# Optimization experiments

Hardware: AMD Instinct MI355X
Metric: run time of the kernel (lower is better)

## Reference

```python
import jax, jax.numpy as jnp
import numpy as np

N, E, T, H, O, L = 8192, 262144, 256, 2048, 1024, 128


def setup_inputs() -> dict:
    key = jax.random.key(0)
    ks = jax.random.split(key, 24)
    inp = {}
    inp["eeg_nodes"] = jax.random.normal(ks[0], (N, T), dtype=jnp.float32)
    inp["eeg_idx"] = jax.random.randint(ks[1], (2, E), 0, N, dtype=jnp.int32)
    # PyG models.GIN layer widths: [T->2048], [2048->2048], [2048->2048], [2048->1024]
    dims = [(T, H), (H, H), (H, H), (H, O)]
    k = 2
    for l, (din, dh) in enumerate(dims):
        inp[f"w1_{l}"] = jax.random.normal(ks[k], (din, dh), jnp.float32) / np.float32(np.sqrt(din)); k += 1
        inp[f"b1_{l}"] = jnp.zeros((dh,), jnp.float32)
        inp[f"w2_{l}"] = jax.random.normal(ks[k], (dh, dh), jnp.float32) / np.float32(np.sqrt(dh)); k += 1
        inp[f"b2_{l}"] = jnp.zeros((dh,), jnp.float32)
    inp["wm"] = jax.random.normal(ks[k], (O, L), jnp.float32) / np.float32(np.sqrt(O)); k += 1
    inp["bm"] = jnp.zeros((L,), jnp.float32)
    inp["wv"] = jax.random.normal(ks[k], (O, L), jnp.float32) / np.float32(np.sqrt(O)); k += 1
    inp["bv"] = jnp.zeros((L,), jnp.float32)
    # reparameterize noise (torch.randn_like) made explicit for determinism
    inp["eps"] = jax.random.normal(ks[k + 1], (N, L), jnp.float32)
    return inp


def _gin_conv(x, src, dst, w1, b1, w2, b2):
    # GINConv, eps=0: mlp((1+0)*x + sum_{j->i} x_j); MLP = Linear-ReLU-Linear (no norm)
    agg = jax.ops.segment_sum(x[src], dst, num_segments=x.shape[0])  # [N, d]
    h = jax.nn.relu((x + agg) @ w1 + b1)
    return h @ w2 + b2


def reference(eeg_nodes, eeg_idx, w1_0, b1_0, w2_0, b2_0, w1_1, b1_1, w2_1, b2_1,
              w1_2, b1_2, w2_2, b2_2, w1_3, b1_3, w2_3, b2_3, wm, bm, wv, bv, eps):
    src, dst = eeg_idx[0], eeg_idx[1]
    layers = [(w1_0, b1_0, w2_0, b2_0), (w1_1, b1_1, w2_1, b2_1),
              (w1_2, b1_2, w2_2, b2_2), (w1_3, b1_3, w2_3, b2_3)]
    x = eeg_nodes
    for i, (w1, b1, w2, b2) in enumerate(layers):
        x = _gin_conv(x, src, dst, w1, b1, w2, b2)
        if i < len(layers) - 1:  # BasicGNN: ReLU between convs, not after last
            x = jax.nn.relu(x)
    mean = x @ wm + bm
    var = x @ wv + bv
    z = mean + var * eps  # reparameterize
    return (z, mean, var)
```

## Files before the change

### kernel.cpp

```cpp
#include <hip/hip_runtime.h>

#define NN 8192
#define EE 262144
#define TT 256
#define HH 2048
#define OO 1024
#define LL 128
#define NW 10

typedef __bf16 bf16_t;
typedef __bf16 bf16x8_t __attribute__((ext_vector_type(8)));
typedef float f32x4_t __attribute__((ext_vector_type(4)));

__device__ __forceinline__ void async16(void* lds, const void* g) {
  __builtin_amdgcn_global_load_lds(
      (const __attribute__((address_space(1))) void*)g,
      (__attribute__((address_space(3))) void*)lds, 16, 0, 0);
}


__global__ __launch_bounds__(256) void count_deg_kernel(const int* __restrict__ dst,
                                                        int* __restrict__ deg) {
  int e = blockIdx.x * 256 + threadIdx.x;
  if (e < EE) atomicAdd(&deg[dst[e]], 1);
}

__global__ __launch_bounds__(1024) void scan_kernel(const int* __restrict__ deg,
                                                    int* __restrict__ rs) {
  __shared__ int s[1024];
  int t = threadIdx.x;
  int pre[8];
  int sum = 0;
#pragma unroll
  for (int j = 0; j < 8; ++j) { pre[j] = sum; sum += deg[t * 8 + j]; }
  s[t] = sum;
  __syncthreads();
  for (int off = 1; off < 1024; off <<= 1) {
    int add = (t >= off) ? s[t - off] : 0;
    __syncthreads();
    s[t] += add;
    __syncthreads();
  }
  int base = (t == 0) ? 0 : s[t - 1];
#pragma unroll
  for (int j = 0; j < 8; ++j) rs[t * 8 + j] = base + pre[j];
  if (t == 1023) rs[8192] = s[1023];
}

__global__ __launch_bounds__(256) void fill_csr_kernel(const int* __restrict__ src,
                                                       const int* __restrict__ dst,
                                                       const int* __restrict__ rs,
                                                       int* __restrict__ cur,
                                                       int* __restrict__ csr) {
  int e = blockIdx.x * 256 + threadIdx.x;
  if (e >= EE) return;
  int d = dst[e];
  int p = atomicAdd(&cur[d], 1);
  csr[rs[d] + p] = src[e];
}

struct WTab {
  const float* src[NW];
  int K[NW];
  int N[NW];
  long long dstOff[NW];
  int tileStart[NW + 1];
  const float* x0;
  bf16_t* castDst;
  int castStart;
};

__global__ __launch_bounds__(256) void prep_all_kernel(WTab tab, bf16_t* __restrict__ WT) {
  int b = blockIdx.x;
  int t = threadIdx.x;
  if (b >= tab.castStart) {
    int i = (b - tab.castStart) * 256 + t;
    f32x4_t a = ((const f32x4_t*)tab.x0)[i * 2];
    f32x4_t bb = ((const f32x4_t*)tab.x0)[i * 2 + 1];
    bf16x8_t o;
#pragma unroll
    for (int j = 0; j < 4; ++j) { o[j] = (bf16_t)a[j]; o[4 + j] = (bf16_t)bb[j]; }
    ((bf16x8_t*)tab.castDst)[i] = o;
    return;
  }
  int wi = 0;
#pragma unroll
  for (int k = 1; k < NW; ++k)
    if (b >= tab.tileStart[k]) wi = k;
  int tt = b - tab.tileStart[wi];
  int K = tab.K[wi], N = tab.N[wi];
  int ntn = N >> 6;
  int n0 = (tt % ntn) * 64, k0 = (tt / ntn) * 64;
  const float* in = tab.src[wi];
  bf16_t* out = WT + tab.dstOff[wi];

  __shared__ float tile[64][65];
  for (int c = t; c < 1024; c += 256) {
    int r = c >> 4, col = (c & 15) * 4;
    f32x4_t v = *(const f32x4_t*)&in[(size_t)(k0 + r) * N + n0 + col];
#pragma unroll
    for (int j = 0; j < 4; ++j) tile[r][col + j] = v[j];
  }
  __syncthreads();
  for (int c = t; c < 512; c += 256) {
    int r = c >> 3, col = (c & 7) * 8;
    bf16x8_t v;
#pragma unroll
    for (int j = 0; j < 8; ++j) v[j] = (bf16_t)tile[col + j][r];
    *(bf16x8_t*)&out[(size_t)(n0 + r) * K + k0 + col] = v;
  }
}

__global__ __launch_bounds__(256) void transpose_cast_kernel(const float* __restrict__ in,
                                                             bf16_t* __restrict__ out,
                                                             int K, int N) {
  __shared__ float tile[64][65];
  int n0 = blockIdx.x * 64, k0 = blockIdx.y * 64;
  int t = threadIdx.x;
  for (int c = t; c < 1024; c += 256) {
    int r = c >> 4, col = (c & 15) * 4;
    f32x4_t v = *(const f32x4_t*)&in[(size_t)(k0 + r) * N + n0 + col];
#pragma unroll
    for (int j = 0; j < 4; ++j) tile[r][col + j] = v[j];
  }
  __syncthreads();
  for (int c = t; c < 512; c += 256) {
    int r = c >> 3, col = (c & 7) * 8;
    bf16x8_t v;
#pragma unroll
    for (int j = 0; j < 8; ++j) v[j] = (bf16_t)tile[col + j][r];
    *(bf16x8_t*)&out[(size_t)(n0 + r) * K + k0 + col] = v;
  }
}

__global__ __launch_bounds__(256) void cast_kernel(const float* __restrict__ in,
                                                   bf16_t* __restrict__ out) {
  int i = blockIdx.x * 256 + threadIdx.x;
  f32x4_t a = ((const f32x4_t*)in)[i * 2];
  f32x4_t b = ((const f32x4_t*)in)[i * 2 + 1];
  bf16x8_t o;
#pragma unroll
  for (int j = 0; j < 4; ++j) { o[j] = (bf16_t)a[j]; o[4 + j] = (bf16_t)b[j]; }
  ((bf16x8_t*)out)[i] = o;
}

__global__ __launch_bounds__(64) void agg0_kernel(const bf16_t* __restrict__ x,
                                                  bf16_t* __restrict__ out,
                                                  const int* __restrict__ rs,
                                                  const int* __restrict__ csr) {
  int t = threadIdx.x;
  int node = blockIdx.x * 2 + (t >> 5);
  int c = t & 31;
  const bf16x8_t* xv = (const bf16x8_t*)x;
  bf16x8_t self = xv[(size_t)node * 32 + c];
  float acc[8];
#pragma unroll
  for (int j = 0; j < 8; ++j) acc[j] = (float)self[j];
  int e0 = rs[node], e1 = rs[node + 1];
  int e = e0;
  for (; e + 4 <= e1; e += 4) {
    int s0 = csr[e], s1 = csr[e + 1], s2 = csr[e + 2], s3 = csr[e + 3];
    bf16x8_t v0 = xv[(size_t)s0 * 32 + c];
    bf16x8_t v1 = xv[(size_t)s1 * 32 + c];
    bf16x8_t v2 = xv[(size_t)s2 * 32 + c];
    bf16x8_t v3 = xv[(size_t)s3 * 32 + c];
#pragma unroll
    for (int j = 0; j < 8; ++j)
      acc[j] += (float)v0[j] + (float)v1[j] + (float)v2[j] + (float)v3[j];
  }
  for (; e < e1; ++e) {
    bf16x8_t v = xv[(size_t)csr[e] * 32 + c];
#pragma unroll
    for (int j = 0; j < 8; ++j) acc[j] += (float)v[j];
  }
  bf16x8_t o;
#pragma unroll
  for (int j = 0; j < 8; ++j) o[j] = (bf16_t)acc[j];
  ((bf16x8_t*)out)[(size_t)node * 32 + c] = o;
}

__global__ __launch_bounds__(256) void agg_tiled_kernel(const bf16_t* __restrict__ x,
                                                        bf16_t* __restrict__ out,
                                                        const int* __restrict__ rs,
                                                        const int* __restrict__ csr,
                                                        const float* __restrict__ bias,
                                                        int relu, int tmask, int tshift) {
  int t = threadIdx.x;
  int tile = blockIdx.x & tmask;
  int ng = blockIdx.x >> tshift;
  int node = ng * 8 + (t >> 5);
  int c = t & 31;
  size_t tb = (size_t)tile * (NN * 32);
  const bf16x8_t* xv = (const bf16x8_t*)x + tb;
  bf16x8_t self = xv[node * 32 + c];
  float acc[8];
#pragma unroll
  for (int j = 0; j < 8; ++j) acc[j] = (float)self[j];
  int e0 = rs[node], e1 = rs[node + 1];
  int e = e0;
  for (; e + 4 <= e1; e += 4) {
    int s0 = csr[e], s1 = csr[e + 1], s2 = csr[e + 2], s3 = csr[e + 3];
    bf16x8_t v0 = xv[s0 * 32 + c];
    bf16x8_t v1 = xv[s1 * 32 + c];
    bf16x8_t v2 = xv[s2 * 32 + c];
    bf16x8_t v3 = xv[s3 * 32 + c];
#pragma unroll
    for (int j = 0; j < 8; ++j)
      acc[j] += (float)v0[j] + (float)v1[j] + (float)v2[j] + (float)v3[j];
  }
  for (; e < e1; ++e) {
    bf16x8_t v = xv[csr[e] * 32 + c];
#pragma unroll
    for (int j = 0; j < 8; ++j) acc[j] += (float)v[j];
  }
  if (bias) {
    const float* bp = bias + tile * 256 + c * 8;
    f32x4_t b0 = *(const f32x4_t*)bp;
    f32x4_t b1 = *(const f32x4_t*)(bp + 4);
#pragma unroll
    for (int j = 0; j < 4; ++j) { acc[j] += b0[j]; acc[4 + j] += b1[j]; }
  }
  if (relu) {
#pragma unroll
    for (int j = 0; j < 8; ++j) acc[j] = fmaxf(acc[j], 0.f);
  }
  bf16x8_t o;
#pragma unroll
  for (int j = 0; j < 8; ++j) o[j] = (bf16_t)acc[j];
  ((bf16x8_t*)out + tb)[node * 32 + c] = o;
}

template <int CMODE>
__global__ __launch_bounds__(256, 2) void gemm_bt_kernel(
    const bf16_t* __restrict__ A, const bf16_t* __restrict__ Bt,
    const float* __restrict__ bias, const float* __restrict__ biasB,
    void* __restrict__ Cv, int N, int K, int relu, int nbxShift) {
  __shared__ __align__(16) bf16_t lA[128 * 32];
  __shared__ __align__(16) bf16_t lB[128 * 32];
  const int tid = threadIdx.x;
  const int lane = tid & 63;
  const int wave = tid >> 6;
  const int wm64 = (wave & 1) * 64;
  const int wn64 = (wave >> 1) * 64;
  const int row16 = lane & 15;
  const int quad = lane >> 4;

  const int bid = blockIdx.x;
  const int xcd = bid & 7;
  const int rank = bid >> 3;
  const int bn = rank & ((1 << nbxShift) - 1);
  const int mPer = gridDim.x >> (3 + nbxShift);
  const int bm = xcd * mPer + (rank >> nbxShift);
  const size_t m0 = (size_t)bm * 128;
  const size_t n0 = (size_t)bn * 128;

  f32x4_t acc[4][4];
#pragma unroll
  for (int i = 0; i < 4; ++i)
#pragma unroll
    for (int j = 0; j < 4; ++j)
#pragma unroll
      for (int r = 0; r < 4; ++r) acc[i][j][r] = 0.f;

  const bf16_t* Bbase = Bt + n0 * K;
  const int r0 = tid >> 2;
  const int r1 = (tid + 256) >> 2;
  const int kc = (tid & 3) * 8;

  for (int kt = 0; kt < K; kt += 32) {
    const bf16_t* Ab = A + ((size_t)(kt >> 8)) * (NN * 256) + (kt & 255) + kc;
    async16(&lA[tid * 8], Ab + (m0 + r0) * 256);
    async16(&lA[(tid + 256) * 8], Ab + (m0 + r1) * 256);
    async16(&lB[tid * 8], Bbase + (size_t)r0 * K + kt + kc);
    async16(&lB[(tid + 256) * 8], Bbase + (size_t)r1 * K + kt + kc);
    __syncthreads();
    bf16x8_t af[4], bfr[4];
#pragma unroll
    for (int i = 0; i < 4; ++i)
      af[i] = *(const bf16x8_t*)&lA[(wm64 + i * 16 + row16) * 32 + quad * 8];
#pragma unroll
    for (int i = 0; i < 4; ++i)
      bfr[i] = *(const bf16x8_t*)&lB[(wn64 + i * 16 + row16) * 32 + quad * 8];
#pragma unroll
    for (int i = 0; i < 4; ++i)
#pragma unroll
      for (int j = 0; j < 4; ++j)
        acc[i][j] = __builtin_amdgcn_mfma_f32_16x16x32_bf16(af[i], bfr[j], acc[i][j], 0, 0, 0);
    __syncthreads();
  }

#pragma unroll
  for (int i = 0; i < 4; ++i) {
    size_t row = m0 + wm64 + i * 16 + quad * 4;
#pragma unroll
    for (int j = 0; j < 4; ++j) {
      int col = (int)n0 + wn64 + j * 16 + row16;
      if (CMODE == 0) {
        float b = bias ? bias[col] : 0.f;
        size_t cb = ((size_t)(col >> 8)) * (NN * 256) + (col & 255);
#pragma unroll
        for (int r = 0; r < 4; ++r) {
          float o = acc[i][j][r] + b;
          if (relu) o = fmaxf(o, 0.f);
          ((bf16_t*)Cv)[cb + (row + r) * 256] = (bf16_t)o;
        }
      } else {
        int sel = col >> 7;
        int c2 = col & 127;
        float b = sel ? biasB[c2] : bias[c2];
        float* dstp = (float*)Cv + (size_t)(1 + sel) * NN * LL + c2;
#pragma unroll
        for (int r = 0; r < 4; ++r) {
          dstp[(row + r) * LL] = acc[i][j][r] + b;
        }
      }
    }
  }
}

__global__ __launch_bounds__(256) void reparam_kernel(const float* __restrict__ mean,
                                                      const float* __restrict__ var,
                                                      const float* __restrict__ eps,
                                                      float* __restrict__ z) {
  int i = blockIdx.x * 256 + threadIdx.x;
  f32x4_t m = ((const f32x4_t*)mean)[i];
  f32x4_t v = ((const f32x4_t*)var)[i];
  f32x4_t e = ((const f32x4_t*)eps)[i];
  f32x4_t o;
#pragma unroll
  for (int j = 0; j < 4; ++j) o[j] = m[j] + v[j] * e[j];
  ((f32x4_t*)z)[i] = o;
}

extern "C" void kernel_launch(void* const* d_in, const int* in_sizes, int n_in,
                              void* d_out, int out_size, void* d_ws, size_t ws_size,
                              hipStream_t stream) {
  (void)in_sizes; (void)n_in; (void)out_size;
  const float* x0 = (const float*)d_in[0];
  const int* ei = (const int*)d_in[1];
  const int* src = ei;
  const int* dst = ei + EE;
  const float* w1[4] = {(const float*)d_in[2], (const float*)d_in[6],
                        (const float*)d_in[10], (const float*)d_in[14]};
  const float* b1[4] = {(const float*)d_in[3], (const float*)d_in[7],
                        (const float*)d_in[11], (const float*)d_in[15]};
  const float* w2[4] = {(const float*)d_in[4], (const float*)d_in[8],
                        (const float*)d_in[12], (const float*)d_in[16]};
  const float* b2[4] = {(const float*)d_in[5], (const float*)d_in[9],
                        (const float*)d_in[13], (const float*)d_in[17]};
  const float* wm = (const float*)d_in[18];
  const float* bm = (const float*)d_in[19];
  const float* wv = (const float*)d_in[20];
  const float* bv = (const float*)d_in[21];
  const float* eps = (const float*)d_in[22];
  float* out = (float*)d_out;

  char* ws = (char*)d_ws;
  bf16_t* B0 = (bf16_t*)(ws);
  bf16_t* B1 = (bf16_t*)(ws + 33554432);
  bf16_t* WT = (bf16_t*)(ws + 67108864);

  const long long soff[NW] = {0LL, 524288LL, 4718592LL, 8912896LL, 13107200LL,
                              17301504LL, 21495808LL, 23592960LL, 24641536LL, 24772608LL};
  const size_t wtBytesFull = 24903680ULL * 2ULL;
  const size_t needFull = 67108864ULL + wtBytesFull + 2097152ULL;
  bool full = ws_size >= needFull;

  size_t csrBase = full ? (67108864ULL + wtBytesFull) : 75497472ULL;
  int* deg = (int*)(ws + csrBase);
  int* cur = deg + 8192;
  int* rs = deg + 16384;
  int* csr = deg + 16384 + 8200;

  auto AGG = [&](const bf16_t* in, bf16_t* outp, int d, const float* bias, int relu) {
    int ntiles = d >> 8;
    int tshift = (ntiles == 8) ? 3 : 2;
    agg_tiled_kernel<<<(NN / 8) * ntiles, 256, 0, stream>>>(in, outp, rs, csr, bias, relu,
                                                            ntiles - 1, tshift);
  };

  if (full) {
    WTab tab;
    const float* srcs[NW] = {w1[0], w2[0], w1[1], w2[1], w1[2], w2[2], w1[3], w2[3], wm, wv};
    const int Ks[NW] = {TT, HH, HH, HH, HH, HH, HH, OO, OO, OO};
    const int Ns[NW] = {HH, HH, HH, HH, HH, HH, OO, OO, LL, LL};
    int cum = 0;
    for (int i = 0; i < NW; ++i) {
      tab.src[i] = srcs[i];
      tab.K[i] = Ks[i];
      tab.N[i] = Ns[i];
      tab.dstOff[i] = soff[i];
      tab.tileStart[i] = cum;
      cum += (Ns[i] >> 6) * (Ks[i] >> 6);
    }
    tab.tileStart[NW] = cum;
    tab.castStart = cum;
    tab.x0 = x0;
    tab.castDst = B0;
    int totalBlocks = cum + (NN * TT / 8) / 256;
    prep_all_kernel<<<totalBlocks, 256, 0, stream>>>(tab, WT);

    hipMemsetAsync(deg, 0, 2 * 8192 * sizeof(int), stream);
    count_deg_kernel<<<EE / 256, 256, 0, stream>>>(dst, deg);
    scan_kernel<<<1, 1024, 0, stream>>>(deg, rs);
    fill_csr_kernel<<<EE / 256, 256, 0, stream>>>(src, dst, rs, cur, csr);

    auto G = [&](const bf16_t* A, int wi, const float* bias, bf16_t* C, int Nn, int K, int relu) {
      int nbx = Nn / 128;
      int shift = __builtin_ctz(nbx);
      gemm_bt_kernel<0><<<nbx * (NN / 128), 256, 0, stream>>>(
          A, WT + soff[wi], bias, nullptr, (void*)C, Nn, K, relu, shift);
    };

    agg0_kernel<<<NN / 2, 64, 0, stream>>>(B0, B1, rs, csr);
    G(B1, 0, b1[0], B0, HH, TT, 1);
    G(B0, 1, b2[0], B1, HH, HH, 1);
    AGG(B1, B0, HH, nullptr, 0);
    G(B0, 2, b1[1], B1, HH, HH, 1);
    G(B1, 3, b2[1], B0, HH, HH, 1);
    AGG(B0, B1, HH, nullptr, 0);
    G(B1, 4, b1[2], B0, HH, HH, 1);
    G(B0, 5, b2[2], B1, HH, HH, 1);
    G(B1, 6, nullptr, B0, OO, HH, 0);
    AGG(B0, B1, OO, b1[3], 1);
    G(B1, 7, b2[3], B0, OO, OO, 0);
    gemm_bt_kernel<1><<<2 * (NN / 128), 256, 0, stream>>>(
        B0, WT + soff[8], bm, bv, (void*)out, 256, OO, 0, 1);
  } else {
    hipMemsetAsync(deg, 0, 2 * 8192 * sizeof(int), stream);
    count_deg_kernel<<<EE / 256, 256, 0, stream>>>(dst, deg);
    scan_kernel<<<1, 1024, 0, stream>>>(deg, rs);
    fill_csr_kernel<<<EE / 256, 256, 0, stream>>>(src, dst, rs, cur, csr);

    auto T = [&](const float* w, int K, int Nn, bf16_t* dstw) {
      transpose_cast_kernel<<<dim3(Nn / 64, K / 64), 256, 0, stream>>>(w, dstw, K, Nn);
    };
    auto G = [&](const bf16_t* A, const float* bias, bf16_t* C, int Nn, int K, int relu) {
      int nbx = Nn / 128;
      int shift = __builtin_ctz(nbx);
      gemm_bt_kernel<0><<<nbx * (NN / 128), 256, 0, stream>>>(
          A, WT, bias, nullptr, (void*)C, Nn, K, relu, shift);
    };

    cast_kernel<<<(NN * TT / 8) / 256, 256, 0, stream>>>(x0, B0);
    agg0_kernel<<<NN / 2, 64, 0, stream>>>(B0, B1, rs, csr);
    T(w1[0], TT, HH, WT); G(B1, b1[0], B0, HH, TT, 1);
    T(w2[0], HH, HH, WT); G(B0, b2[0], B1, HH, HH, 1);
    AGG(B1, B0, HH, nullptr, 0);
    T(w1[1], HH, HH, WT); G(B0, b1[1], B1, HH, HH, 1);
    T(w2[1], HH, HH, WT); G(B1, b2[1], B0, HH, HH, 1);
    AGG(B0, B1, HH, nullptr, 0);
    T(w1[2], HH, HH, WT); G(B1, b1[2], B0, HH, HH, 1);
    T(w2[2], HH, HH, WT); G(B0, b2[2], B1, HH, HH, 1);
    T(w1[3], HH, OO, WT); G(B1, nullptr, B0, OO, HH, 0);
    AGG(B0, B1, OO, b1[3], 1);
    T(w2[3], OO, OO, WT); G(B1, b2[3], B0, OO, OO, 0);
    T(wm, OO, LL, WT);
    T(wv, OO, LL, WT + (size_t)LL * OO);
    gemm_bt_kernel<1><<<2 * (NN / 128), 256, 0, stream>>>(
        B0, WT, bm, bv, (void*)out, 256, OO, 0, 1);
  }

  reparam_kernel<<<(NN * LL / 4) / 256, 256, 0, stream>>>(
      out + (size_t)NN * LL, out + (size_t)2 * NN * LL, eps, out);
}
```

Measured before the change: 874.2 us.

## Add 256x256-tile 8-wave GEMM with quadrant ping-pong for 2048-wide layers

Adds a new GEMM kernel that uses 256x256 output tiles with 512 threads, double-buffered LDS, and a four-quadrant schedule interleaving LDS fragment loads, async global-to-LDS staging and MFMA blocks with priority raising. It replaces the 128x128 GEMM for all six N=2048 layers. The aim is higher arithmetic intensity per loaded byte and better overlap of memory with matrix cores. In exchange it uses 128 KB of LDS per block, heavy register pressure, and a fine-grained barrier schedule whose correctness depends on precise vmcnt accounting.

```diff
diff --git a/kernel.cpp b/kernel.cpp
--- a/kernel.cpp
+++ b/kernel.cpp
@@ -316,6 +316,155 @@
       }
     }
   }
+}
+
+__global__ __launch_bounds__(512, 2) void gemm256_kernel(
+    const bf16_t* __restrict__ A, const bf16_t* __restrict__ Bt,
+    const float* __restrict__ bias, bf16_t* __restrict__ C,
+    int N, int K, int relu, int nbxShift) {
+  __shared__ __align__(16) bf16_t lA[2][256 * 64];
+  __shared__ __align__(16) bf16_t lB[2][256 * 64];
+
+  const int t = threadIdx.x;
+  const int lane = t & 63;
+  const int wave = t >> 6;
+  const int wm = wave >> 2;
+  const int wn = wave & 3;
+  const int row16 = lane & 15;
+  const int quad = lane >> 4;
+  const int sx = (row16 & 7) << 3;
+
+  const int r0 = t >> 3;
+  const int cs = ((t & 7) * 8) ^ ((r0 & 7) << 3);
+
+  const int bid = blockIdx.x;
+  const int xcd = bid & 7;
+  const int rank = bid >> 3;
+  const int bn = rank & ((1 << nbxShift) - 1);
+  const int mPer = gridDim.x >> (3 + nbxShift);
+  const int bm = xcd * mPer + (rank >> nbxShift);
+  const size_t m0 = (size_t)bm * 256;
+  const size_t n0 = (size_t)bn * 256;
+  const int NT = K >> 6;
+
+  f32x4_t acc[4][4][2];
+#pragma unroll
+  for (int Q = 0; Q < 4; ++Q)
+#pragma unroll
+    for (int i = 0; i < 4; ++i)
+#pragma unroll
+      for (int j = 0; j < 2; ++j)
+#pragma unroll
+        for (int r = 0; r < 4; ++r) acc[Q][i][j][r] = 0.f;
+
+  bf16x8_t af[4][2], bf[2][2];
+
+#define LOAD_A256(mh)                                                              \
+  _Pragma("unroll") for (int i = 0; i < 4; ++i)                                    \
+  _Pragma("unroll") for (int ks = 0; ks < 2; ++ks) {                               \
+    int row_ = (mh)*128 + wm * 64 + i * 16 + row16;                                \
+    af[i][ks] = *(const bf16x8_t*)&lA[c][row_ * 64 + ((ks * 32 + quad * 8) ^ sx)]; \
+  }
+
+#define LOAD_B256(nh)                                                              \
+  _Pragma("unroll") for (int j = 0; j < 2; ++j)                                    \
+  _Pragma("unroll") for (int ks = 0; ks < 2; ++ks) {                               \
+    int row_ = (nh)*128 + wn * 32 + j * 16 + row16;                                \
+    bf[j][ks] = *(const bf16x8_t*)&lB[c][row_ * 64 + ((ks * 32 + quad * 8) ^ sx)]; \
+  }
+
+#define STAGE_A256(U, mh)                                                            \
+  {                                                                                  \
+    int u_ = (U);                                                                    \
+    int us_ = u_ < NT ? u_ : NT - 1;                                                 \
+    int kt_ = us_ << 6;                                                              \
+    const bf16_t* g_ = A + (size_t)(kt_ >> 8) * (NN * 256) + (m0 + (mh)*128) * 256 + \
+                       (kt_ & 255) + cs;                                             \
+    bf16_t* l_ = &lA[u_ & 1][(mh)*8192];                                             \
+    async16(l_ + (size_t)t * 8, g_ + (size_t)r0 * 256);                              \
+    async16(l_ + (size_t)(t + 512) * 8, g_ + (size_t)(r0 + 64) * 256);               \
+  }
+
+#define STAGE_B256(U, nh)                                                  \
+  {                                                                        \
+    int u_ = (U);                                                          \
+    int us_ = u_ < NT ? u_ : NT - 1;                                       \
+    int kt_ = us_ << 6;                                                    \
+    const bf16_t* g_ = Bt + (n0 + (nh)*128) * (size_t)K + kt_ + cs;        \
+    bf16_t* l_ = &lB[u_ & 1][(nh)*8192];                                   \
+    async16(l_ + (size_t)t * 8, g_ + (size_t)r0 * K);                      \
+    async16(l_ + (size_t)(t + 512) * 8, g_ + (size_t)(r0 + 64) * K);       \
+  }
+
+#define MFMA_Q(Q)                                                                    \
+  __builtin_amdgcn_s_setprio(1);                                                     \
+  _Pragma("unroll") for (int i = 0; i < 4; ++i)                                      \
+  _Pragma("unroll") for (int j = 0; j < 2; ++j)                                      \
+  _Pragma("unroll") for (int ks = 0; ks < 2; ++ks)                                   \
+      acc[Q][i][j] =                                                                 \
+          __builtin_amdgcn_mfma_f32_16x16x32_bf16(af[i][ks], bf[j][ks], acc[Q][i][j],\
+                                                  0, 0, 0);                          \
+  __builtin_amdgcn_s_setprio(0);
+
+#define BAR asm volatile("s_barrier" ::: "memory")
+
+  STAGE_A256(0, 0); STAGE_B256(0, 0); STAGE_A256(0, 1); STAGE_B256(0, 1);
+  asm volatile("" ::: "memory");
+  STAGE_A256(1, 0); STAGE_B256(1, 0);
+  asm volatile("s_waitcnt vmcnt(4)" ::: "memory");
+  BAR;
+
+  for (int T = 0; T < NT; ++T) {
+    const int c = T & 1;
+    LOAD_A256(0); LOAD_B256(0);
+    STAGE_A256(T + 1, 1); STAGE_B256(T + 1, 1);
+    BAR;
+    MFMA_Q(0);
+    BAR;
+    LOAD_B256(1);
+    BAR;
+    MFMA_Q(1);
+    BAR;
+    LOAD_A256(1); LOAD_B256(0);
+    STAGE_A256(T + 2, 0);
+    BAR;
+    MFMA_Q(2);
+    BAR;
+    LOAD_B256(1);
+    STAGE_B256(T + 2, 0);
+    BAR;
+    MFMA_Q(3);
+    asm volatile("s_waitcnt vmcnt(4)" ::: "memory");
+    BAR;
+  }
+  asm volatile("s_waitcnt vmcnt(0)" ::: "memory");
+
+#pragma unroll
+  for (int Q = 0; Q < 4; ++Q) {
+    const int mh = Q >> 1, nh = Q & 1;
+#pragma unroll
+    for (int i = 0; i < 4; ++i) {
+      size_t row = m0 + mh * 128 + wm * 64 + i * 16 + quad * 4;
+#pragma unroll
+      for (int j = 0; j < 2; ++j) {
+        int col = (int)n0 + nh * 128 + wn * 32 + j * 16 + row16;
+        float b = bias ? bias[col] : 0.f;
+        size_t cb = ((size_t)(col >> 8)) * (NN * 256) + (col & 255);
+#pragma unroll
+        for (int r = 0; r < 4; ++r) {
+          float o = acc[Q][i][j][r] + b;
+          if (relu) o = fmaxf(o, 0.f);
+          C[cb + (row + r) * 256] = (bf16_t)o;
+        }
+      }
+    }
+  }
+#undef LOAD_A256
+#undef LOAD_B256
+#undef STAGE_A256
+#undef STAGE_B256
+#undef MFMA_Q
+#undef BAR
 }
 
 __global__ __launch_bounds__(256) void reparam_kernel(const float* __restrict__ mean,
@@ -405,22 +554,27 @@
     scan_kernel<<<1, 1024, 0, stream>>>(deg, rs);
     fill_csr_kernel<<<EE / 256, 256, 0, stream>>>(src, dst, rs, cur, csr);
 
-    auto G = [&](const bf16_t* A, int wi, const float* bias, bf16_t* C, int Nn, int K, int relu) {
+    auto G2 = [&](const bf16_t* Ain, int wi, const float* bias, bf16_t* Cout, int K, int relu) {
+      gemm256_kernel<<<8 * (NN / 256), 512, 0, stream>>>(Ain, WT + soff[wi], bias, Cout,
+                                                         HH, K, relu, 3);
+    };
+    auto G = [&](const bf16_t* Ain, int wi, const float* bias, bf16_t* Cout, int Nn, int K,
+                 int relu) {
       int nbx = Nn / 128;
       int shift = __builtin_ctz(nbx);
       gemm_bt_kernel<0><<<nbx * (NN / 128), 256, 0, stream>>>(
-          A, WT + soff[wi], bias, nullptr, (void*)C, Nn, K, relu, shift);
+          Ain, WT + soff[wi], bias, nullptr, (void*)Cout, Nn, K, relu, shift);
     };
 
     agg0_kernel<<<NN / 2, 64, 0, stream>>>(B0, B1, rs, csr);
-    G(B1, 0, b1[0], B0, HH, TT, 1);
-    G(B0, 1, b2[0], B1, HH, HH, 1);
+    G2(B1, 0, b1[0], B0, TT, 1);
+    G2(B0, 1, b2[0], B1, HH, 1);
     AGG(B1, B0, HH, nullptr, 0);
-    G(B0, 2, b1[1], B1, HH, HH, 1);
-    G(B1, 3, b2[1], B0, HH, HH, 1);
+    G2(B0, 2, b1[1], B1, HH, 1);
+    G2(B1, 3, b2[1], B0, HH, 1);
     AGG(B0, B1, HH, nullptr, 0);
-    G(B1, 4, b1[2], B0, HH, HH, 1);
-    G(B0, 5, b2[2], B1, HH, HH, 1);
+    G2(B1, 4, b1[2], B0, HH, 1);
+    G2(B0, 5, b2[2], B1, HH, 1);
     G(B1, 6, nullptr, B0, OO, HH, 0);
     AGG(B0, B1, OO, b1[3], 1);
     G(B1, 7, b2[3], B0, OO, OO, 0);
@@ -435,23 +589,26 @@
     auto T = [&](const float* w, int K, int Nn, bf16_t* dstw) {
       transpose_cast_kernel<<<dim3(Nn / 64, K / 64), 256, 0, stream>>>(w, dstw, K, Nn);
     };
-    auto G = [&](const bf16_t* A, const float* bias, bf16_t* C, int Nn, int K, int relu) {
+    auto G2 = [&](const bf16_t* Ain, const float* bias, bf16_t* Cout, int K, int relu) {
+      gemm256_kernel<<<8 * (NN / 256), 512, 0, stream>>>(Ain, WT, bias, Cout, HH, K, relu, 3);
+    };
+    auto G = [&](const bf16_t* Ain, const float* bias, bf16_t* Cout, int Nn, int K, int relu) {
       int nbx = Nn / 128;
       int shift = __builtin_ctz(nbx);
       gemm_bt_kernel<0><<<nbx * (NN / 128), 256, 0, stream>>>(
-          A, WT, bias, nullptr, (void*)C, Nn, K, relu, shift);
+          Ain, WT, bias, nullptr, (void*)Cout, Nn, K, relu, shift);
     };
 
     cast_kernel<<<(NN * TT / 8) / 256, 256, 0, stream>>>(x0, B0);
     agg0_kernel<<<NN / 2, 64, 0, stream>>>(B0, B1, rs, csr);
-    T(w1[0], TT, HH, WT); G(B1, b1[0], B0, HH, TT, 1);
-    T(w2[0], HH, HH, WT); G(B0, b2[0], B1, HH, HH, 1);
+    T(w1[0], TT, HH, WT); G2(B1, b1[0], B0, TT, 1);
+    T(w2[0], HH, HH, WT); G2(B0, b2[0], B1, HH, 1);
     AGG(B1, B0, HH, nullptr, 0);
-    T(w1[1], HH, HH, WT); G(B0, b1[1], B1, HH, HH, 1);
-    T(w2[1], HH, HH, WT); G(B1, b2[1], B0, HH, HH, 1);
+    T(w1[1], HH, HH, WT); G2(B0, b1[1], B1, HH, 1);
+    T(w2[1], HH, HH, WT); G2(B1, b2[1], B0, HH, 1);
     AGG(B0, B1, HH, nullptr, 0);
-    T(w1[2], HH, HH, WT); G(B1, b1[2], B0, HH, HH, 1);
-    T(w2[2], HH, HH, WT); G(B0, b2[2], B1, HH, HH, 1);
+    T(w1[2], HH, HH, WT); G2(B1, b1[2], B0, HH, 1);
+    T(w2[2], HH, HH, WT); G2(B0, b2[2], B1, HH, 1);
     T(w1[3], HH, OO, WT); G(B1, nullptr, B0, OO, HH, 0);
     AGG(B0, B1, OO, b1[3], 1);
     T(w2[3], OO, OO, WT); G(B1, b2[3], B0, OO, OO, 0);
```

Measured after the change: 812.1 us. 1.08x faster.
